# Kernel tuning notes

Measured on AMD Instinct MI355X. Metric: run time of the kernel, lower is better.

## Reference

```python
import jax, jax.numpy as jnp
import numpy as np
import math

B, LT, LS, D, H, DFF = 2, 2048, 2048, 1024, 16, 4096
DK = D // H


def layer_norm(x, g, b, eps=1e-5):
    mu = jnp.mean(x, axis=-1, keepdims=True)
    var = jnp.var(x, axis=-1, keepdims=True)
    return (x - mu) * jax.lax.rsqrt(var + eps) * g + b


def mha(q_in, k_in, v_in, wq, bq, wk, bk, wv, bv, wo, bo, mask):
    Bq, Lq, _ = q_in.shape
    Lk = k_in.shape[1]
    Q = (q_in @ wq + bq).reshape(Bq, Lq, H, DK).transpose(0, 2, 1, 3)
    K = (k_in @ wk + bk).reshape(Bq, Lk, H, DK).transpose(0, 2, 1, 3)
    V = (v_in @ wv + bv).reshape(Bq, Lk, H, DK).transpose(0, 2, 1, 3)
    scores = jnp.einsum('bhqd,bhkd->bhqk', Q, K) / math.sqrt(DK)  # [B,H,Lq,Lk]
    if mask is not None:
        scores = jnp.where(mask == 0, jnp.float32(-1e9), scores)
    attn = jax.nn.softmax(scores, axis=-1)
    out = jnp.einsum('bhqk,bhkd->bhqd', attn, V)
    out = out.transpose(0, 2, 1, 3).reshape(Bq, Lq, D)
    return out @ wo + bo


def setup_inputs() -> dict:
    key = jax.random.key(0)
    ks = jax.random.split(key, 24)
    s = 0.02
    inp = {
        'x': jax.random.normal(ks[0], (B, LT, D), jnp.float32),
        'encoder_output': jax.random.normal(ks[1], (B, LS, D), jnp.float32),
        'tgt_mask': jnp.tril(jnp.ones((LT, LT), jnp.int32)),  # causal
        'src_mask': jnp.ones((B, 1, 1, LS), jnp.int32),       # all-valid padding mask
    }
    names = ['self_wq', 'self_wk', 'self_wv', 'self_wo',
             'cross_wq', 'cross_wk', 'cross_wv', 'cross_wo']
    for i, n in enumerate(names):
        inp[n] = jax.random.normal(ks[2 + i], (D, D), jnp.float32) * s
        inp[n.replace('w', 'b')] = jnp.zeros((D,), jnp.float32)
    inp['ff_w1'] = jax.random.normal(ks[10], (D, DFF), jnp.float32) * s
    inp['ff_b1'] = jnp.zeros((DFF,), jnp.float32)
    inp['ff_w2'] = jax.random.normal(ks[11], (DFF, D), jnp.float32) * s
    inp['ff_b2'] = jnp.zeros((D,), jnp.float32)
    for i, n in enumerate(['n1', 'n2', 'n3']):
        inp[n + '_g'] = jnp.ones((D,), jnp.float32)
        inp[n + '_b'] = jnp.zeros((D,), jnp.float32)
    return inp


def reference(x, encoder_output, tgt_mask, src_mask,
              self_wq, self_bq, self_wk, self_bk, self_wv, self_bv, self_wo, self_bo,
              cross_wq, cross_bq, cross_wk, cross_bk, cross_wv, cross_bv, cross_wo, cross_bo,
              ff_w1, ff_b1, ff_w2, ff_b2,
              n1_g, n1_b, n2_g, n2_b, n3_g, n3_b):
    # dropout is identity (eval mode)
    attn_out = mha(x, x, x, self_wq, self_bq, self_wk, self_bk,
                   self_wv, self_bv, self_wo, self_bo, tgt_mask)
    x = layer_norm(x + attn_out, n1_g, n1_b)
    attn_out = mha(x, encoder_output, encoder_output, cross_wq, cross_bq,
                   cross_wk, cross_bk, cross_wv, cross_bv, cross_wo, cross_bo, src_mask)
    x = layer_norm(x + attn_out, n2_g, n2_b)
    ff_out = (jax.nn.gelu(x @ ff_w1 + ff_b1, approximate=False)) @ ff_w2 + ff_b2
    x = layer_norm(x + ff_out, n3_g, n3_b)
    return x
```

## Files before the change

kernel.cpp:

```cpp
#include <hip/hip_runtime.h>
#include <cstdint>
#include <math.h>


typedef unsigned short u16;
typedef __attribute__((ext_vector_type(8))) short bf16x8;
typedef __attribute__((ext_vector_type(4))) float f32x4;
typedef __attribute__((ext_vector_type(8))) unsigned short u16x8;
typedef __attribute__((ext_vector_type(4))) unsigned short u16x4;

__device__ __forceinline__ float b2f(u16 h) {
  return __uint_as_float(((unsigned)h) << 16);
}
__device__ __forceinline__ u16 f2b(float f) {
  unsigned u = __float_as_uint(f);
  u += 0x7fffu + ((u >> 16) & 1u);
  return (u16)(u >> 16);
}
__device__ __forceinline__ f32x4 mfma16x16x32(bf16x8 a, bf16x8 b, f32x4 c) {
  return __builtin_amdgcn_mfma_f32_16x16x32_bf16(a, b, c, 0, 0, 0);
}
__device__ __forceinline__ void gld16(const u16* g, u16* l) {
  __builtin_amdgcn_global_load_lds(
      (const __attribute__((address_space(1))) void*)g,
      (__attribute__((address_space(3))) void*)l, 16, 0, 0);
}
__device__ __forceinline__ float ldv(const void* p, int i, int f32m) {
  return f32m ? ((const float*)p)[i] : b2f(((const u16*)p)[i]);
}

__global__ void detect_k(const unsigned* __restrict__ g, int* __restrict__ flag) {
  if (threadIdx.x == 0 && blockIdx.x == 0)
    *flag = (g[0] == 0x3F800000u) ? 1 : 0;
}

__global__ __launch_bounds__(256) void convert_in(
    const void* __restrict__ src, u16* __restrict__ dst,
    const int* __restrict__ flag, int n) {
  const int i = (blockIdx.x * 256 + threadIdx.x) * 8;
  if (i >= n) return;
  if (*flag) {
    const float4* s4 = (const float4*)((const float*)src + i);
    float4 v0 = s4[0], v1 = s4[1];
    u16x8 o;
    o[0] = f2b(v0.x); o[1] = f2b(v0.y); o[2] = f2b(v0.z); o[3] = f2b(v0.w);
    o[4] = f2b(v1.x); o[5] = f2b(v1.y); o[6] = f2b(v1.z); o[7] = f2b(v1.w);
    *(u16x8*)(dst + i) = o;
  } else {
    *(u16x8*)(dst + i) = *(const u16x8*)((const u16*)src + i);
  }
}

__global__ __launch_bounds__(256) void transpose_k(
    const void* __restrict__ Sv, u16* __restrict__ D,
    const int* __restrict__ flag, int R, int C) {
  __shared__ u16 t[32][33];
  const int c0 = blockIdx.x * 32, r0 = blockIdx.y * 32;
  const int tid = threadIdx.x;
  const int r = tid >> 3, c4 = (tid & 7) << 2;
  u16 e0, e1, e2, e3;
  if (*flag) {
    const float* S = (const float*)Sv;
    float4 v = *(const float4*)(S + (size_t)(r0 + r) * C + c0 + c4);
    e0 = f2b(v.x); e1 = f2b(v.y); e2 = f2b(v.z); e3 = f2b(v.w);
  } else {
    const u16* S = (const u16*)Sv;
    u16x4 v = *(const u16x4*)(S + (size_t)(r0 + r) * C + c0 + c4);
    e0 = v[0]; e1 = v[1]; e2 = v[2]; e3 = v[3];
  }
  t[r][c4 + 0] = e0; t[r][c4 + 1] = e1;
  t[r][c4 + 2] = e2; t[r][c4 + 3] = e3;
  __syncthreads();
  u16x4 o;
  o[0] = t[c4 + 0][r]; o[1] = t[c4 + 1][r];
  o[2] = t[c4 + 2][r]; o[3] = t[c4 + 3][r];
  *(u16x4*)(D + (size_t)(c0 + r) * R + r0 + c4) = o;
}

template <int MODE, bool ACT>
__global__ __launch_bounds__(256) void gemm_bt(
    const u16* __restrict__ A, const u16* __restrict__ Bt,
    const void* __restrict__ bias0, const void* __restrict__ bias1,
    const void* __restrict__ bias2, const int* __restrict__ flagp,
    u16* __restrict__ out0, u16* __restrict__ out1, u16* __restrict__ out2,
    int M, int N, int K) {
  __shared__ __align__(16) u16 As[128 * 32];
  __shared__ __align__(16) u16 Bs[128 * 32];
  const int tid = threadIdx.x;
  const int w = tid >> 6, lane = tid & 63;
  const int quad = lane >> 4, l16 = lane & 15;
  const int m0 = blockIdx.y << 7, n0 = blockIdx.x << 7;
  const int wm = (w >> 1) << 6, wn = (w & 1) << 6;

  const f32x4 zero = {0.f, 0.f, 0.f, 0.f};
  f32x4 acc[4][4];
#pragma unroll
  for (int i = 0; i < 4; ++i)
#pragma unroll
    for (int j = 0; j < 4; ++j) acc[i][j] = zero;

  const int c1 = tid, c2 = tid + 256;
  const int r1 = c1 >> 2, k1o = (c1 & 3) << 3;
  const int r2 = c2 >> 2, k2o = (c2 & 3) << 3;
  const u16* ag1 = A + (size_t)(m0 + r1) * K + k1o;
  const u16* ag2 = A + (size_t)(m0 + r2) * K + k2o;
  const u16* bg1 = Bt + (size_t)(n0 + r1) * K + k1o;
  const u16* bg2 = Bt + (size_t)(n0 + r2) * K + k2o;
  u16* As1 = As + (w << 9);
  u16* As2 = As + 2048 + (w << 9);
  u16* Bs1 = Bs + (w << 9);
  u16* Bs2 = Bs + 2048 + (w << 9);
  const u16* apl = As + (wm + l16) * 32 + (quad << 3);
  const u16* bpl = Bs + (wn + l16) * 32 + (quad << 3);

  const int KT = K >> 5;
  for (int kt = 0; kt < KT; ++kt) {
    gld16(ag1, As1); gld16(ag2, As2);
    gld16(bg1, Bs1); gld16(bg2, Bs2);
    ag1 += 32; ag2 += 32; bg1 += 32; bg2 += 32;
    __syncthreads();
    bf16x8 af[4], bfr[4];
#pragma unroll
    for (int i = 0; i < 4; ++i) af[i] = *(const bf16x8*)(apl + (i << 9));
#pragma unroll
    for (int j = 0; j < 4; ++j) bfr[j] = *(const bf16x8*)(bpl + (j << 9));
#pragma unroll
    for (int i = 0; i < 4; ++i)
#pragma unroll
      for (int j = 0; j < 4; ++j)
        acc[i][j] = mfma16x16x32(af[i], bfr[j], acc[i][j]);
    __syncthreads();
  }

  const int f32m = *flagp;
#pragma unroll
  for (int i = 0; i < 4; ++i) {
    const int rbase = m0 + wm + (i << 4) + (quad << 2);
#pragma unroll
    for (int j = 0; j < 4; ++j) {
      const int col = n0 + wn + (j << 4) + l16;
      int nm, dd;
      if (MODE == 0 || MODE == 3) { nm = 0; dd = col; }
      else { nm = col >> 10; dd = col & 1023; }
      const void* bp = (nm == 0) ? bias0 : ((nm == 1) ? bias1 : bias2);
      const float bv = ldv(bp, dd, f32m);
#pragma unroll
      for (int r = 0; r < 4; ++r) {
        float v = acc[i][j][r] + bv;
        if (ACT) v = 0.5f * v * (1.f + erff(v * 0.70710678f));
        const int m = rbase + r;
        if (MODE == 0) {
          out0[(size_t)m * N + col] = f2b(v);
        } else {
          const int hh = dd >> 6, dk = dd & 63;
          const int bb = m >> 11, ss = m & 2047;
          u16* op; bool vt;
          if (MODE == 1) { op = (nm == 0) ? out0 : ((nm == 1) ? out1 : out2); vt = (nm == 2); }
          else if (MODE == 2) { op = (nm == 0) ? out0 : out1; vt = (nm == 1); }
          else { op = out0; vt = false; }
          const size_t a = vt
              ? ((((size_t)bb * 16 + hh) * 64 + dk) * 2048 + ss)
              : ((((size_t)bb * 16 + hh) * 2048 + ss) * 64 + dk);
          op[a] = f2b(v);
        }
      }
    }
  }
}

__global__ __launch_bounds__(256) void flash_attn(
    const u16* __restrict__ Qp, const u16* __restrict__ Kp,
    const u16* __restrict__ VTp, u16* __restrict__ Op,
    int L, int causal) {
  __shared__ __align__(16) u16 P[4][16 * 144];
  const int tid = threadIdx.x;
  const int w = tid >> 6, lane = tid & 63;
  const int quad = lane >> 4, l16 = lane & 15;
  const int bh = blockIdx.y;
  const int qb = blockIdx.x << 6;
  const int qbase = qb + (w << 4);
  const size_t hoff = (size_t)bh * L * 64;
  const u16* Kh = Kp + hoff;
  const u16* VTh = VTp + hoff;
  const u16* qptr = Qp + hoff + (size_t)(qbase + l16) * 64 + (quad << 3);
  bf16x8 qf0 = *(const bf16x8*)(qptr);
  bf16x8 qf1 = *(const bf16x8*)(qptr + 32);
  const f32x4 zero = {0.f, 0.f, 0.f, 0.f};
  f32x4 ov[4];
#pragma unroll
  for (int d = 0; d < 4; ++d) ov[d] = zero;
  float mrow[4], lrow[4];
#pragma unroll
  for (int r = 0; r < 4; ++r) { mrow[r] = -INFINITY; lrow[r] = 0.f; }
  u16* Pw = &P[w][0];
  const int qrow0 = qbase + (quad << 2);
  const int nch = causal ? ((qb >> 7) + 1) : (L >> 7);

  for (int t = 0; t < nch; ++t) {
    const int kt0 = t << 7;
    float sv[8][4];
#pragma unroll
    for (int st = 0; st < 8; ++st) {
      const u16* kp = Kh + (size_t)(kt0 + (st << 4) + l16) * 64 + (quad << 3);
      bf16x8 kf0 = *(const bf16x8*)(kp);
      bf16x8 kf1 = *(const bf16x8*)(kp + 32);
      f32x4 sa = mfma16x16x32(qf1, kf1, mfma16x16x32(qf0, kf0, zero));
      const int kc = kt0 + (st << 4) + l16;
#pragma unroll
      for (int r = 0; r < 4; ++r) {
        float xv = sa[r] * 0.125f;
        if (causal && (kc > qrow0 + r)) xv = -1e30f;
        sv[st][r] = xv;
      }
    }
    float tm[4];
#pragma unroll
    for (int r = 0; r < 4; ++r) {
      float a = fmaxf(fmaxf(sv[0][r], sv[1][r]), fmaxf(sv[2][r], sv[3][r]));
      float b = fmaxf(fmaxf(sv[4][r], sv[5][r]), fmaxf(sv[6][r], sv[7][r]));
      tm[r] = fmaxf(a, b);
    }
#pragma unroll
    for (int d = 1; d < 16; d <<= 1)
#pragma unroll
      for (int r = 0; r < 4; ++r) tm[r] = fmaxf(tm[r], __shfl_xor(tm[r], d));
    float alpha[4], rs[4];
#pragma unroll
    for (int r = 0; r < 4; ++r) {
      const float mn = fmaxf(mrow[r], tm[r]);
      alpha[r] = exp2f((mrow[r] - mn) * 1.44269504f);
      mrow[r] = mn;
      float a = 0.f;
#pragma unroll
      for (int st = 0; st < 8; ++st) {
        const float p = exp2f((sv[st][r] - mn) * 1.44269504f);
        sv[st][r] = p;
        a += p;
      }
      rs[r] = a;
    }
#pragma unroll
    for (int d = 1; d < 16; d <<= 1)
#pragma unroll
      for (int r = 0; r < 4; ++r) rs[r] += __shfl_xor(rs[r], d);
#pragma unroll
    for (int r = 0; r < 4; ++r) lrow[r] = lrow[r] * alpha[r] + rs[r];
#pragma unroll
    for (int dd = 0; dd < 4; ++dd)
#pragma unroll
      for (int r = 0; r < 4; ++r) ov[dd][r] *= alpha[r];
    __threadfence_block();
#pragma unroll
    for (int st = 0; st < 8; ++st)
#pragma unroll
      for (int r = 0; r < 4; ++r)
        Pw[((quad << 2) + r) * 144 + (st << 4) + l16] = f2b(sv[st][r]);
    __threadfence_block();
    bf16x8 pf[4];
#pragma unroll
    for (int q = 0; q < 4; ++q)
      pf[q] = *(const bf16x8*)(Pw + l16 * 144 + (q << 5) + (quad << 3));
#pragma unroll
    for (int dd = 0; dd < 4; ++dd) {
      const u16* vp = VTh + (size_t)((dd << 4) + l16) * L + kt0 + (quad << 3);
      bf16x8 vf0 = *(const bf16x8*)(vp);
      bf16x8 vf1 = *(const bf16x8*)(vp + 32);
      bf16x8 vf2 = *(const bf16x8*)(vp + 64);
      bf16x8 vf3 = *(const bf16x8*)(vp + 96);
      ov[dd] = mfma16x16x32(pf[0], vf0, ov[dd]);
      ov[dd] = mfma16x16x32(pf[1], vf1, ov[dd]);
      ov[dd] = mfma16x16x32(pf[2], vf2, ov[dd]);
      ov[dd] = mfma16x16x32(pf[3], vf3, ov[dd]);
    }
  }
  const int b = bh >> 4, h = bh & 15;
#pragma unroll
  for (int dd = 0; dd < 4; ++dd) {
#pragma unroll
    for (int r = 0; r < 4; ++r) {
      const int q = qrow0 + r;
      const size_t a = ((size_t)b * L + q) * 1024 + (h << 6) + (dd << 4) + l16;
      Op[a] = f2b(ov[dd][r] / lrow[r]);
    }
  }
}

template <bool DYN_OUT>
__global__ __launch_bounds__(256) void add_ln(
    const u16* __restrict__ X, const u16* __restrict__ Y,
    const void* __restrict__ G, const void* __restrict__ Bi,
    const int* __restrict__ flagp, void* __restrict__ O) {
  const int tid = threadIdx.x;
  const int w = tid >> 6, lane = tid & 63;
  const size_t row = (size_t)blockIdx.x * 4 + w;
  const size_t base = row * 1024 + (size_t)lane * 16;
  const int f32m = *flagp;
  u16x8 xa = *(const u16x8*)(X + base);
  u16x8 xb = *(const u16x8*)(X + base + 8);
  u16x8 ya = *(const u16x8*)(Y + base);
  u16x8 yb = *(const u16x8*)(Y + base + 8);
  float v[16];
  float s = 0.f, sq = 0.f;
#pragma unroll
  for (int j = 0; j < 8; ++j) {
    v[j] = b2f(xa[j]) + b2f(ya[j]);
    v[8 + j] = b2f(xb[j]) + b2f(yb[j]);
  }
#pragma unroll
  for (int j = 0; j < 16; ++j) { s += v[j]; sq += v[j] * v[j]; }
#pragma unroll
  for (int d = 1; d < 64; d <<= 1) {
    s += __shfl_xor(s, d);
    sq += __shfl_xor(sq, d);
  }
  const float mu = s * (1.f / 1024.f);
  const float var = sq * (1.f / 1024.f) - mu * mu;
  const float rstd = rsqrtf(var + 1e-5f);
  const int go = lane * 16;
  float o[16];
#pragma unroll
  for (int j = 0; j < 16; ++j)
    o[j] = (v[j] - mu) * rstd * ldv(G, go + j, f32m) + ldv(Bi, go + j, f32m);
  if (DYN_OUT && f32m) {
    float4* op = (float4*)((float*)O + base);
#pragma unroll
    for (int j = 0; j < 4; ++j) {
      float4 q; q.x = o[j * 4]; q.y = o[j * 4 + 1]; q.z = o[j * 4 + 2]; q.w = o[j * 4 + 3];
      op[j] = q;
    }
  } else {
    u16x8 oa, ob;
#pragma unroll
    for (int j = 0; j < 8; ++j) { oa[j] = f2b(o[j]); ob[j] = f2b(o[8 + j]); }
    *(u16x8*)((u16*)O + base) = oa;
    *(u16x8*)((u16*)O + base + 8) = ob;
  }
}

extern "C" void kernel_launch(void* const* d_in, const int* in_sizes, int n_in,
                              void* d_out, int out_size, void* d_ws, size_t ws_size,
                              hipStream_t stream) {
  (void)in_sizes; (void)n_in; (void)out_size; (void)ws_size;
  const void* x   = d_in[0];
  const void* enc = d_in[1];
  const void* swq = d_in[4];  const void* sbq = d_in[5];
  const void* swk = d_in[6];  const void* sbk = d_in[7];
  const void* swv = d_in[8];  const void* sbv = d_in[9];
  const void* swo = d_in[10]; const void* sbo = d_in[11];
  const void* cwq = d_in[12]; const void* cbq = d_in[13];
  const void* cwk = d_in[14]; const void* cbk = d_in[15];
  const void* cwv = d_in[16]; const void* cbv = d_in[17];
  const void* cwo = d_in[18]; const void* cbo = d_in[19];
  const void* fw1 = d_in[20]; const void* fb1 = d_in[21];
  const void* fw2 = d_in[22]; const void* fb2 = d_in[23];
  const void* n1g = d_in[24]; const void* n1b = d_in[25];
  const void* n2g = d_in[26]; const void* n2b = d_in[27];
  const void* n3g = d_in[28]; const void* n3b = d_in[29];

  const size_t MM = 1024 * 1024;
  u16* W = (u16*)d_ws;
  u16* wqkvT = W;
  u16* wosT  = W + 3 * MM;
  u16* wqcT  = W + 4 * MM;
  u16* wkvcT = W + 5 * MM;
  u16* wocT  = W + 7 * MM;
  u16* wf1T  = W + 8 * MM;
  u16* wf2T  = W + 12 * MM;
  u16* xb    = W + 16 * MM;
  u16* encb  = W + 20 * MM;
  u16* Qb    = W + 24 * MM;
  u16* Kb    = W + 28 * MM;
  u16* VTb   = W + 32 * MM;
  u16* attn  = W + 36 * MM;
  u16* x1    = W + 40 * MM;
  u16* tmp   = W + 44 * MM;
  u16* ffh   = Kb;
  u16* x2    = Qb;
  int* flag  = (int*)(W + 48 * MM);

  const dim3 blk(256);
  detect_k<<<dim3(1), dim3(64), 0, stream>>>((const unsigned*)n1g, flag);

  convert_in<<<dim3(2048), blk, 0, stream>>>(x, xb, flag, 4 * MM);
  convert_in<<<dim3(2048), blk, 0, stream>>>(enc, encb, flag, 4 * MM);

  transpose_k<<<dim3(32, 32), blk, 0, stream>>>(swq, wqkvT,          flag, 1024, 1024);
  transpose_k<<<dim3(32, 32), blk, 0, stream>>>(swk, wqkvT + MM,     flag, 1024, 1024);
  transpose_k<<<dim3(32, 32), blk, 0, stream>>>(swv, wqkvT + 2 * MM, flag, 1024, 1024);
  transpose_k<<<dim3(32, 32), blk, 0, stream>>>(swo, wosT,           flag, 1024, 1024);
  transpose_k<<<dim3(32, 32), blk, 0, stream>>>(cwq, wqcT,           flag, 1024, 1024);
  transpose_k<<<dim3(32, 32), blk, 0, stream>>>(cwk, wkvcT,          flag, 1024, 1024);
  transpose_k<<<dim3(32, 32), blk, 0, stream>>>(cwv, wkvcT + MM,     flag, 1024, 1024);
  transpose_k<<<dim3(32, 32), blk, 0, stream>>>(cwo, wocT,           flag, 1024, 1024);
  transpose_k<<<dim3(128, 32), blk, 0, stream>>>(fw1, wf1T, flag, 1024, 4096);
  transpose_k<<<dim3(32, 128), blk, 0, stream>>>(fw2, wf2T, flag, 4096, 1024);

  gemm_bt<1, false><<<dim3(24, 32), blk, 0, stream>>>(
      xb, wqkvT, sbq, sbk, sbv, flag, Qb, Kb, VTb, 4096, 3072, 1024);
  flash_attn<<<dim3(32, 32), blk, 0, stream>>>(Qb, Kb, VTb, attn, 2048, 1);
  gemm_bt<0, false><<<dim3(8, 32), blk, 0, stream>>>(
      attn, wosT, sbo, nullptr, nullptr, flag, tmp, nullptr, nullptr, 4096, 1024, 1024);
  add_ln<false><<<dim3(1024), blk, 0, stream>>>(xb, tmp, n1g, n1b, flag, x1);

  gemm_bt<3, false><<<dim3(8, 32), blk, 0, stream>>>(
      x1, wqcT, cbq, nullptr, nullptr, flag, Qb, nullptr, nullptr, 4096, 1024, 1024);
  gemm_bt<2, false><<<dim3(16, 32), blk, 0, stream>>>(
      encb, wkvcT, cbk, cbv, nullptr, flag, Kb, VTb, nullptr, 4096, 2048, 1024);
  flash_attn<<<dim3(32, 32), blk, 0, stream>>>(Qb, Kb, VTb, attn, 2048, 0);
  gemm_bt<0, false><<<dim3(8, 32), blk, 0, stream>>>(
      attn, wocT, cbo, nullptr, nullptr, flag, tmp, nullptr, nullptr, 4096, 1024, 1024);
  add_ln<false><<<dim3(1024), blk, 0, stream>>>(x1, tmp, n2g, n2b, flag, x2);

  gemm_bt<0, true><<<dim3(32, 32), blk, 0, stream>>>(
      x2, wf1T, fb1, nullptr, nullptr, flag, ffh, nullptr, nullptr, 4096, 4096, 1024);
  gemm_bt<0, false><<<dim3(8, 32), blk, 0, stream>>>(
      ffh, wf2T, fb2, nullptr, nullptr, flag, tmp, nullptr, nullptr, 4096, 1024, 4096);
  add_ln<true><<<dim3(1024), blk, 0, stream>>>(x2, tmp, n3g, n3b, flag, d_out);
}
```

Before: 1.072 ms.

## Split attention KV range across two wave groups with LDS merge

Flash attention blocks become 512 threads: two groups of four waves each take half of the key chunks for the same 64 query rows. The partial outputs and the row max and sum statistics are then merged through shared memory. This doubles parallelism per query tile and shortens each wave's serial KV loop. It also applies the causal mask only on the diagonal chunks, swaps the thread fences for compiler barriers, and changes the LDS padding. In exchange it adds a __syncthreads and extra LDS traffic for the merge, and the causal split gives the two halves unequal work on short rows.

```diff
diff --git a/kernel.cpp b/kernel.cpp
--- a/kernel.cpp
+++ b/kernel.cpp
@@ -168,17 +168,19 @@
   }
 }
 
-__global__ __launch_bounds__(256) void flash_attn(
+__global__ __launch_bounds__(512, 8) void flash_attn(
     const u16* __restrict__ Qp, const u16* __restrict__ Kp,
     const u16* __restrict__ VTp, u16* __restrict__ Op,
     int L, int causal) {
-  __shared__ __align__(16) u16 P[4][16 * 144];
+  __shared__ __align__(16) u16 P[8][16 * 136];
+  __shared__ float ML[4][16][2];
   const int tid = threadIdx.x;
   const int w = tid >> 6, lane = tid & 63;
+  const int half = w >> 2, w4 = w & 3;
   const int quad = lane >> 4, l16 = lane & 15;
   const int bh = blockIdx.y;
   const int qb = blockIdx.x << 6;
-  const int qbase = qb + (w << 4);
+  const int qbase = qb + (w4 << 4);
   const size_t hoff = (size_t)bh * L * 64;
   const u16* Kh = Kp + hoff;
   const u16* VTh = VTp + hoff;
@@ -195,8 +197,11 @@
   u16* Pw = &P[w][0];
   const int qrow0 = qbase + (quad << 2);
   const int nch = causal ? ((qb >> 7) + 1) : (L >> 7);
-
-  for (int t = 0; t < nch; ++t) {
+  const int mid = (nch + 1) >> 1;
+  const int t0 = half ? mid : 0;
+  const int t1 = half ? nch : mid;
+
+  for (int t = t0; t < t1; ++t) {
     const int kt0 = t << 7;
     float sv[8][4];
 #pragma unroll
@@ -205,12 +210,16 @@
       bf16x8 kf0 = *(const bf16x8*)(kp);
       bf16x8 kf1 = *(const bf16x8*)(kp + 32);
       f32x4 sa = mfma16x16x32(qf1, kf1, mfma16x16x32(qf0, kf0, zero));
-      const int kc = kt0 + (st << 4) + l16;
-#pragma unroll
-      for (int r = 0; r < 4; ++r) {
-        float xv = sa[r] * 0.125f;
-        if (causal && (kc > qrow0 + r)) xv = -1e30f;
-        sv[st][r] = xv;
+#pragma unroll
+      for (int r = 0; r < 4; ++r) sv[st][r] = sa[r] * 0.125f;
+    }
+    if (causal && (kt0 + 127 > qbase)) {
+#pragma unroll
+      for (int st = 0; st < 8; ++st) {
+        const int kc = kt0 + (st << 4) + l16;
+#pragma unroll
+        for (int r = 0; r < 4; ++r)
+          if (kc > qrow0 + r) sv[st][r] = -1e30f;
       }
     }
     float tm[4];
@@ -249,17 +258,17 @@
     for (int dd = 0; dd < 4; ++dd)
 #pragma unroll
       for (int r = 0; r < 4; ++r) ov[dd][r] *= alpha[r];
-    __threadfence_block();
+    __asm__ volatile("" ::: "memory");
 #pragma unroll
     for (int st = 0; st < 8; ++st)
 #pragma unroll
       for (int r = 0; r < 4; ++r)
-        Pw[((quad << 2) + r) * 144 + (st << 4) + l16] = f2b(sv[st][r]);
-    __threadfence_block();
+        Pw[((quad << 2) + r) * 136 + (st << 4) + l16] = f2b(sv[st][r]);
+    __asm__ volatile("" ::: "memory");
     bf16x8 pf[4];
 #pragma unroll
     for (int q = 0; q < 4; ++q)
-      pf[q] = *(const bf16x8*)(Pw + l16 * 144 + (q << 5) + (quad << 3));
+      pf[q] = *(const bf16x8*)(Pw + l16 * 136 + (q << 5) + (quad << 3));
 #pragma unroll
     for (int dd = 0; dd < 4; ++dd) {
       const u16* vp = VTh + (size_t)((dd << 4) + l16) * L + kt0 + (quad << 3);
@@ -273,14 +282,46 @@
       ov[dd] = mfma16x16x32(pf[3], vf3, ov[dd]);
     }
   }
-  const int b = bh >> 4, h = bh & 15;
-#pragma unroll
-  for (int dd = 0; dd < 4; ++dd) {
+
+  if (half) {
+    float* mb = (float*)&P[w][0];
+#pragma unroll
+    for (int dd = 0; dd < 4; ++dd)
+#pragma unroll
+      for (int r = 0; r < 4; ++r)
+        mb[((quad << 2) + r) * 68 + (dd << 4) + l16] = ov[dd][r];
+    if (l16 == 0) {
+#pragma unroll
+      for (int r = 0; r < 4; ++r) {
+        ML[w4][(quad << 2) + r][0] = mrow[r];
+        ML[w4][(quad << 2) + r][1] = lrow[r];
+      }
+    }
+  }
+  __syncthreads();
+  if (!half) {
+    const float* pb = (const float*)&P[w4 + 4][0];
+    float al1[4], al2[4], inv[4];
 #pragma unroll
     for (int r = 0; r < 4; ++r) {
-      const int q = qrow0 + r;
-      const size_t a = ((size_t)b * L + q) * 1024 + (h << 6) + (dd << 4) + l16;
-      Op[a] = f2b(ov[dd][r] / lrow[r]);
+      const float m2 = ML[w4][(quad << 2) + r][0];
+      const float l2 = ML[w4][(quad << 2) + r][1];
+      const float M = fmaxf(mrow[r], m2);
+      al1[r] = exp2f((mrow[r] - M) * 1.44269504f);
+      al2[r] = exp2f((m2 - M) * 1.44269504f);
+      inv[r] = 1.f / (lrow[r] * al1[r] + l2 * al2[r]);
+    }
+    const int b = bh >> 4, h = bh & 15;
+#pragma unroll
+    for (int dd = 0; dd < 4; ++dd) {
+#pragma unroll
+      for (int r = 0; r < 4; ++r) {
+        const float o2 = pb[((quad << 2) + r) * 68 + (dd << 4) + l16];
+        const float o = (ov[dd][r] * al1[r] + o2 * al2[r]) * inv[r];
+        const int q = qrow0 + r;
+        const size_t a = ((size_t)b * L + q) * 1024 + (h << 6) + (dd << 4) + l16;
+        Op[a] = f2b(o);
+      }
     }
   }
 }
@@ -397,7 +438,7 @@
 
   gemm_bt<1, false><<<dim3(24, 32), blk, 0, stream>>>(
       xb, wqkvT, sbq, sbk, sbv, flag, Qb, Kb, VTb, 4096, 3072, 1024);
-  flash_attn<<<dim3(32, 32), blk, 0, stream>>>(Qb, Kb, VTb, attn, 2048, 1);
+  flash_attn<<<dim3(32, 32), dim3(512), 0, stream>>>(Qb, Kb, VTb, attn, 2048, 1);
   gemm_bt<0, false><<<dim3(8, 32), blk, 0, stream>>>(
       attn, wosT, sbo, nullptr, nullptr, flag, tmp, nullptr, nullptr, 4096, 1024, 1024);
   add_ln<false><<<dim3(1024), blk, 0, stream>>>(xb, tmp, n1g, n1b, flag, x1);
@@ -406,7 +447,7 @@
       x1, wqcT, cbq, nullptr, nullptr, flag, Qb, nullptr, nullptr, 4096, 1024, 1024);
   gemm_bt<2, false><<<dim3(16, 32), blk, 0, stream>>>(
       encb, wkvcT, cbk, cbv, nullptr, flag, Kb, VTb, nullptr, 4096, 2048, 1024);
-  flash_attn<<<dim3(32, 32), blk, 0, stream>>>(Qb, Kb, VTb, attn, 2048, 0);
+  flash_attn<<<dim3(32, 32), dim3(512), 0, stream>>>(Qb, Kb, VTb, attn, 2048, 0);
   gemm_bt<0, false><<<dim3(8, 32), blk, 0, stream>>>(
       attn, wocT, cbo, nullptr, nullptr, flag, tmp, nullptr, nullptr, 4096, 1024, 1024);
   add_ln<false><<<dim3(1024), blk, 0, stream>>>(x1, tmp, n2g, n2b, flag, x2);
```

Result: slower. 1.328 ms (+23.9%).
